# Kernel tuning notes

Measured on AMD Instinct MI355X. Metric: run time of the kernel, lower is better.

The kernel has to match this reference:

```python
import jax, jax.numpy as jnp
import numpy as np

SEQ_LEN, BATCH, VOCAB, EMB, HID, NUM_LAYERS = 128, 64, 10000, 512, 512, 2


def setup_inputs() -> dict:
    key = jax.random.key(0)
    ks = jax.random.split(key, 16)
    b = float(np.sqrt(1.0 / HID))  # Linear init bound per init_weights_uniform
    u = lambda k, shape, bound: jax.random.uniform(k, shape, jnp.float32, -bound, bound)
    L = NUM_LAYERS - 1
    return {
        "inputs": jax.random.randint(ks[0], (SEQ_LEN, BATCH), 0, VOCAB, dtype=jnp.int32),
        "hidden": jnp.zeros((NUM_LAYERS, BATCH, HID), jnp.float32),
        "emb": u(ks[1], (VOCAB, EMB), 0.1),
        "W_ih0": u(ks[2], (HID, EMB), b),
        "b_ih0": u(ks[3], (HID,), b),
        "W_hh0": u(ks[4], (HID, HID), b),
        "b_hh0": u(ks[5], (HID,), b),
        "W_in": u(ks[6], (L, HID, HID), b),
        "b_in": u(ks[7], (L, HID), b),
        "W_hh": u(ks[8], (L, HID, HID), b),
        "b_hh": u(ks[9], (L, HID), b),
        "Wy": u(ks[10], (VOCAB, HID), 0.1),
        "by": jnp.zeros((VOCAB,), jnp.float32),
    }


def reference(inputs, hidden, emb, W_ih0, b_ih0, W_hh0, b_hh0,
              W_in, b_in, W_hh, b_hh, Wy, by):
    n_extra = W_in.shape[0]  # num_layers - 1 (static)

    def step(h, x_t):
        # h: [L, B, H]; x_t: [B] int tokens
        e = emb[x_t]  # [B, E]
        h0 = jnp.tanh(e @ W_ih0.T + b_ih0 + h[0] @ W_hh0.T + b_hh0)
        hs = [h0]
        for l in range(n_extra):  # small static layer loop
            hl = jnp.tanh(hs[-1] @ W_in[l].T + b_in[l]
                          + h[l + 1] @ W_hh[l].T + b_hh[l])
            hs.append(hl)
        h_new = jnp.stack(hs)  # [L, B, H]
        logits_t = hs[-1] @ Wy.T + by  # [B, V]
        return h_new, logits_t

    hidden_final, logits = jax.lax.scan(step, hidden, inputs)
    return logits, hidden_final  # [S, B, V], [L, B, H]
```

## Files before the change

kernel.cpp:

```cpp
#include <hip/hip_runtime.h>
#include <hip/hip_bf16.h>

#define SEQ 128
#define BAT 64
#define VOC 10000
#define EMBD 512
#define HID 512
#define BH (BAT*HID)
#define PRE0_OFF 0
#define H0_OFF   ((size_t)SEQ*BH)
#define H1_OFF   (H0_OFF + (size_t)(SEQ+1)*BH)
#define FLAGS_OFF (H1_OFF + (size_t)(SEQ+1)*BH)
#define CONV_OFF (FLAGS_OFF + 256)
#define LOGITS_N ((size_t)SEQ*BAT*VOC)
#define CONV_USHORTS 5382144ull
#define WS_NEED_FLOATS (CONV_OFF + CONV_USHORTS/2)

typedef __attribute__((ext_vector_type(8))) __bf16 bf16x8;
typedef __attribute__((ext_vector_type(4))) float f32x4;

__global__ __launch_bounds__(256) void init_state_k(const float* __restrict__ hidden,
                                                    float* __restrict__ h0_0,
                                                    float* __restrict__ h1_0,
                                                    unsigned* __restrict__ flags) {
    int i = blockIdx.x * 256 + threadIdx.x;
    if (i < 256) flags[i] = 0u;
    if (i < BH) { h0_0[i] = hidden[i]; h1_0[i] = hidden[BH + i]; }
}

__global__ __launch_bounds__(256) void gemm_nt_k(
    const float* __restrict__ A, const int* __restrict__ tok,
    const float* __restrict__ Bm,
    const float* __restrict__ bias0, const float* __restrict__ bias1,
    float* __restrict__ C, int N, int K, int ldc)
{
    __shared__ float As[32][132];
    __shared__ float Bs[32][132];
    __shared__ int toks[128];

    const int tid = threadIdx.x;
    const int r0 = blockIdx.x * 128;
    const int c0 = blockIdx.y * 128;

    if (tok != nullptr && tid < 128) toks[tid] = tok[r0 + tid];
    __syncthreads();

    const int tn = tid & 15;
    const int tm = tid >> 4;
    const int m0 = tm * 8, n0 = tn * 8;

    float acc[8][8];
#pragma unroll
    for (int i = 0; i < 8; ++i)
#pragma unroll
        for (int j = 0; j < 8; ++j) acc[i][j] = 0.f;

    for (int k0 = 0; k0 < K; k0 += 32) {
#pragma unroll
        for (int p = 0; p < 4; ++p) {
            int idx = p * 256 + tid;
            int row = idx >> 3;
            int kq  = (idx & 7) << 2;
            size_t arow = tok ? (size_t)toks[row] : (size_t)(r0 + row);
            float4 a = *(const float4*)(A + arow * (size_t)K + k0 + kq);
            As[kq+0][row] = a.x; As[kq+1][row] = a.y;
            As[kq+2][row] = a.z; As[kq+3][row] = a.w;
            int gc = c0 + row;
            float4 b = make_float4(0.f, 0.f, 0.f, 0.f);
            if (gc < N) b = *(const float4*)(Bm + (size_t)gc * K + k0 + kq);
            Bs[kq+0][row] = b.x; Bs[kq+1][row] = b.y;
            Bs[kq+2][row] = b.z; Bs[kq+3][row] = b.w;
        }
        __syncthreads();
#pragma unroll 8
        for (int k = 0; k < 32; ++k) {
            float4 a0 = *(const float4*)&As[k][m0];
            float4 a1 = *(const float4*)&As[k][m0 + 4];
            float4 b0 = *(const float4*)&Bs[k][n0];
            float4 b1 = *(const float4*)&Bs[k][n0 + 4];
            float am[8] = {a0.x,a0.y,a0.z,a0.w,a1.x,a1.y,a1.z,a1.w};
            float bn[8] = {b0.x,b0.y,b0.z,b0.w,b1.x,b1.y,b1.z,b1.w};
#pragma unroll
            for (int i = 0; i < 8; ++i)
#pragma unroll
                for (int j = 0; j < 8; ++j) acc[i][j] += am[i] * bn[j];
        }
        __syncthreads();
    }

    const bool full = (c0 + 128 <= N);
#pragma unroll
    for (int i = 0; i < 8; ++i) {
        size_t r = (size_t)(r0 + m0 + i);
        float* crow = C + r * (size_t)ldc;
#pragma unroll
        for (int j = 0; j < 8; ++j) {
            int c = c0 + n0 + j;
            if (full || c < N) {
                float v = acc[i][j];
                if (bias0) v += bias0[c];
                if (bias1) v += bias1[c];
                crow[c] = v;
            }
        }
    }
}

#define BFLY(S, N)                                                     \
    {                                                                  \
        _Pragma("unroll")                                              \
        for (int i = 0; i < N; ++i) {                                  \
            float lo_ = a[i], hi_ = a[i + N];                          \
            float send_ = (lane & S) ? lo_ : hi_;                      \
            float recv_ = __shfl_xor(send_, S);                       \
            a[i] = ((lane & S) ? hi_ : lo_) + recv_;                   \
        }                                                              \
    }

__device__ __forceinline__ unsigned bf16_rne(float x) {
    unsigned u = __float_as_uint(x);
    unsigned r = u + 0x7fffu + ((u >> 16) & 1u);
    return r >> 16;
}

__device__ __forceinline__ void recurrence_body(
    int blk,
    const float* __restrict__ pre0, const float* __restrict__ W_hh0,
    const float* __restrict__ W_in, const float* __restrict__ b_in,
    const float* __restrict__ W_hh, const float* __restrict__ b_hh,
    float* __restrict__ h0_all, float* __restrict__ h1_all,
    unsigned* __restrict__ flags, float* __restrict__ xs)
{
    const int tid  = threadIdx.x;
    const int lane = tid & 63;
    const int wv   = tid >> 6;
    const int p = ((lane&1)<<5)|((lane&2)<<3)|((lane&4)<<1)
                | ((lane&8)>>1)|((lane&16)>>3)|((lane&32)>>5);
    const int b_own = p >> 3, j_own = p & 7;

    unsigned* fl1 = flags;
    unsigned* fl2 = flags + 64;

    float4 wr[8][2];
    float a[64];

    if (blk < 64) {
        const int g = blk >> 4, jb = blk & 15;
        const int bt = wv & 1, jt = wv >> 1;
        const size_t win = (size_t)(g << 4) * HID;
#pragma unroll
        for (int jj = 0; jj < 8; ++jj) {
            const float* wp = W_hh0 + (size_t)(jb*32 + jt*8 + jj) * HID;
            wr[jj][0] = *(const float4*)(wp + lane*4);
            wr[jj][1] = *(const float4*)(wp + 256 + lane*4);
        }
        const unsigned* grp = fl1 + (g << 4);
        unsigned* myf = fl1 + (g << 4) + jb;
        const int bg = (g << 4) + (bt << 3) + b_own;
        const int jg = jb*32 + jt*8 + j_own;

        for (unsigned t = 1; t <= SEQ; ++t) {
            float pf = pre0[(size_t)(t-1)*BH + (size_t)bg*HID + jg];
            for (;;) {
                unsigned v = __hip_atomic_load(&grp[lane & 15], __ATOMIC_RELAXED,
                                               __HIP_MEMORY_SCOPE_AGENT);
                if (__ballot(v < (t - 1)) == 0ull) break;
            }
            __syncthreads();
            {
                const float4* src = (const float4*)(h0_all + (size_t)(t-1)*BH + win);
                float4 r0_, r1_, r2_, r3_;
                asm volatile("global_load_dwordx4 %0, %1, off sc0" : "=v"(r0_) : "v"(src + tid));
                asm volatile("global_load_dwordx4 %0, %1, off sc0" : "=v"(r1_) : "v"(src + tid + 512));
                asm volatile("global_load_dwordx4 %0, %1, off sc0" : "=v"(r2_) : "v"(src + tid + 1024));
                asm volatile("global_load_dwordx4 %0, %1, off sc0" : "=v"(r3_) : "v"(src + tid + 1536));
                asm volatile("s_waitcnt vmcnt(0)" ::: "memory");
                __builtin_amdgcn_sched_barrier(0);
                float4* dst = (float4*)xs;
                dst[tid] = r0_; dst[tid+512] = r1_; dst[tid+1024] = r2_; dst[tid+1536] = r3_;
            }
            __syncthreads();
#pragma unroll
            for (int i = 0; i < 64; ++i) a[i] = 0.f;
#pragma unroll
            for (int b = 0; b < 8; ++b) {
                const int row = (bt << 3) + b;
                float4 ha = *(const float4*)&xs[row*512 + lane*4];
                float4 hb = *(const float4*)&xs[row*512 + 256 + lane*4];
#pragma unroll
                for (int jj = 0; jj < 8; ++jj) {
                    a[b*8+jj] += ha.x*wr[jj][0].x + ha.y*wr[jj][0].y
                               + ha.z*wr[jj][0].z + ha.w*wr[jj][0].w
                               + hb.x*wr[jj][1].x + hb.y*wr[jj][1].y
                               + hb.z*wr[jj][1].z + hb.w*wr[jj][1].w;
                }
            }
            BFLY(1,32) BFLY(2,16) BFLY(4,8) BFLY(8,4) BFLY(16,2) BFLY(32,1)
            float v = tanhf(a[0] + pf);
            __hip_atomic_store(&h0_all[(size_t)t*BH + (size_t)bg*HID + jg], v,
                               __ATOMIC_RELAXED, __HIP_MEMORY_SCOPE_AGENT);
            asm volatile("s_waitcnt vmcnt(0)" ::: "memory");
            __syncthreads();
            if (tid == 0) __hip_atomic_store(myf, t, __ATOMIC_RELAXED,
                                             __HIP_MEMORY_SCOPE_AGENT);
        }
    } else {
        const int idx = blk - 64;
        const int g = idx >> 5, jb = idx & 31;
        const int bt = wv & 1, jt = (wv >> 1) & 1, kt = wv >> 2;
        const size_t win = (size_t)(g << 4) * HID;
        const float* Wmat = kt ? W_hh : W_in;
#pragma unroll
        for (int jj = 0; jj < 8; ++jj) {
            const float* wp = Wmat + (size_t)(jb*16 + jt*8 + jj) * HID;
            wr[jj][0] = *(const float4*)(wp + lane*4);
            wr[jj][1] = *(const float4*)(wp + 256 + lane*4);
        }
        const unsigned* grpA = fl1 + (g << 4);
        const unsigned* grpB = fl2 + (g << 5);
        unsigned* myf = fl2 + (g << 5) + jb;
        const int bg = (g << 4) + (bt << 3) + b_own;
        const int jg = jb*16 + jt*8 + j_own;
        const float bias = b_in[jg] + b_hh[jg];
        const int scx = (wv & 3) * 64 + lane;

        for (unsigned t = 1; t <= SEQ; ++t) {
            for (;;) {
                unsigned v1 = __hip_atomic_load(&grpA[lane & 15], __ATOMIC_RELAXED,
                                                __HIP_MEMORY_SCOPE_AGENT);
                unsigned v2 = __hip_atomic_load(&grpB[lane & 31], __ATOMIC_RELAXED,
                                                __HIP_MEMORY_SCOPE_AGENT);
                if (__ballot(v1 < t) == 0ull && __ballot(v2 < (t - 1)) == 0ull) break;
            }
            __syncthreads();
            {
                const int q = tid & 255;
                const float4* src = (tid < 256)
                    ? (const float4*)(h0_all + (size_t)t*BH + win)
                    : (const float4*)(h1_all + (size_t)(t-1)*BH + win);
                float4 rr[8];
#pragma unroll
                for (int i = 0; i < 8; ++i)
                    asm volatile("global_load_dwordx4 %0, %1, off sc0"
                                 : "=v"(rr[i]) : "v"(src + q + i*256));
                asm volatile("s_waitcnt vmcnt(0)" ::: "memory");
                __builtin_amdgcn_sched_barrier(0);
                float4* dst = (float4*)(xs + ((tid < 256) ? 0 : 8192));
#pragma unroll
                for (int i = 0; i < 8; ++i) dst[q + i*256] = rr[i];
            }
            __syncthreads();
#pragma unroll
            for (int i = 0; i < 64; ++i) a[i] = 0.f;
            const float* xsrc = xs + (kt ? 8192 : 0);
#pragma unroll
            for (int b = 0; b < 8; ++b) {
                const int row = (bt << 3) + b;
                float4 ha = *(const float4*)&xsrc[row*512 + lane*4];
                float4 hb = *(const float4*)&xsrc[row*512 + 256 + lane*4];
#pragma unroll
                for (int jj = 0; jj < 8; ++jj) {
                    a[b*8+jj] += ha.x*wr[jj][0].x + ha.y*wr[jj][0].y
                               + ha.z*wr[jj][0].z + ha.w*wr[jj][0].w
                               + hb.x*wr[jj][1].x + hb.y*wr[jj][1].y
                               + hb.z*wr[jj][1].z + hb.w*wr[jj][1].w;
                }
            }
            BFLY(1,32) BFLY(2,16) BFLY(4,8) BFLY(8,4) BFLY(16,2) BFLY(32,1)
            __syncthreads();
            if (kt) xs[scx] = a[0];
            __syncthreads();
            if (!kt) {
                float v = tanhf(a[0] + xs[scx] + bias);
                __hip_atomic_store(&h1_all[(size_t)t*BH + (size_t)bg*HID + jg], v,
                                   __ATOMIC_RELAXED, __HIP_MEMORY_SCOPE_AGENT);
            }
            asm volatile("s_waitcnt vmcnt(0)" ::: "memory");
            __syncthreads();
            if (tid == 0) __hip_atomic_store(myf, t, __ATOMIC_RELAXED,
                                             __HIP_MEMORY_SCOPE_AGENT);
        }
    }
}

__global__ __launch_bounds__(512) void recurrence_k(
    const float* __restrict__ pre0, const float* __restrict__ W_hh0,
    const float* __restrict__ W_in, const float* __restrict__ b_in,
    const float* __restrict__ W_hh, const float* __restrict__ b_hh,
    float* __restrict__ h0_all, float* __restrict__ h1_all,
    unsigned* __restrict__ flags)
{
    __shared__ float xs[16384];
    recurrence_body(blockIdx.x, pre0, W_hh0, W_in, b_in, W_hh, b_hh,
                    h0_all, h1_all, flags, xs);
}

__global__ __launch_bounds__(512, 2) void recurrence9_k(
    const float* __restrict__ pre0, const float* __restrict__ W_hh0,
    const float* __restrict__ W_in, const float* __restrict__ b_in,
    const float* __restrict__ W_hh, const float* __restrict__ b_hh,
    float* __restrict__ h0_all, float* __restrict__ h1_all,
    unsigned* __restrict__ flags)
{
    __shared__ float xs[16384];
    __shared__ int s_task;

    if (threadIdx.x == 0) {
        unsigned xcc;
        asm volatile("s_getreg_b32 %0, hwreg(20, 0, 4)" : "=s"(xcc));
        unsigned* q = flags + 192;
        int task = -1;
        if (xcc < 4u) {
            unsigned r = atomicAdd(&q[xcc], 1u);
            if (r < 48u) task = (r < 16u) ? (int)(xcc*16u + r)
                                          : (int)(64u + xcc*32u + (r - 16u));
        }
        if (task < 0) {
            __builtin_amdgcn_s_sleep(127);
            for (unsigned g = 0; g < 4u && task < 0; ++g) {
                unsigned r = atomicAdd(&q[g], 1u);
                if (r < 48u) task = (r < 16u) ? (int)(g*16u + r)
                                              : (int)(64u + g*32u + (r - 16u));
            }
        }
        s_task = task;
    }
    __syncthreads();
    const int task = s_task;
    if (task < 0) return;

    recurrence_body(task, pre0, W_hh0, W_in, b_in, W_hh, b_hh,
                    h0_all, h1_all, flags, xs);
}

__global__ __launch_bounds__(256) void copy_out_k(const float* __restrict__ h0_all,
                                                  const float* __restrict__ h1_all,
                                                  float* __restrict__ out_hidden) {
    int g = blockIdx.x * 256 + threadIdx.x;
    if (g < BH)            out_hidden[g] = h0_all[(size_t)SEQ * BH + g];
    else if (g < 2 * BH)   out_hidden[g] = h1_all[(size_t)SEQ * BH + (g - BH)];
}


__global__ __launch_bounds__(256) void split2_hi_k(const float* __restrict__ wy,
                                                   const float* __restrict__ wih0,
                                                   unsigned short* __restrict__ wy_hi,
                                                   unsigned short* __restrict__ wih0_hi) {
    const int n4a = VOC*HID/4;
    const int n4b = HID*EMBD/4;
    int i = blockIdx.x * 256 + threadIdx.x;
    const float* src; unsigned short* dst; int idx;
    if (i < n4a)            { src = wy;   dst = wy_hi;   idx = i; }
    else if (i < n4a + n4b) { src = wih0; dst = wih0_hi; idx = i - n4a; }
    else return;
    float4 v = ((const float4*)src)[idx];
    ushort4 h4;
    h4.x = (unsigned short)bf16_rne(v.x); h4.y = (unsigned short)bf16_rne(v.y);
    h4.z = (unsigned short)bf16_rne(v.z); h4.w = (unsigned short)bf16_rne(v.w);
    ((ushort4*)dst)[idx] = h4;
}

__global__ __launch_bounds__(256) void gemm_mfma2f_k(
    const float* __restrict__ Ag, const int* __restrict__ tok,
    const unsigned short* __restrict__ Bhg,
    const float* __restrict__ bias0, const float* __restrict__ bias1,
    float* __restrict__ C, int N, int ldc)
{
    __shared__ __align__(16) unsigned short sAh[128*64];
    __shared__ __align__(16) unsigned short sAl[128*64];
    __shared__ __align__(16) unsigned short sBh[128*64];

    const int tid = threadIdx.x;
    const int flat = blockIdx.y * gridDim.x + blockIdx.x;
    const int cpx  = (gridDim.x * gridDim.y) >> 3;
    const int w    = (flat & 7) * cpx + (flat >> 3);
    const int r0 = (w & 63) * 128, c0 = (w >> 6) * 128;

    const int lane = tid & 63, wvv = tid >> 6;
    const int mh = wvv >> 1, nh = wvv & 1;

    f32x4 acc[4][4];
#pragma unroll
    for (int i = 0; i < 4; ++i)
#pragma unroll
        for (int j = 0; j < 4; ++j) acc[i][j] = (f32x4){0.f, 0.f, 0.f, 0.f};

    const int srow = tid >> 1, shalf = tid & 1;
    const size_t arow = tok ? (size_t)tok[r0 + srow] : (size_t)(r0 + srow);
    const size_t abase = arow * 512 + (size_t)shalf * 32;
    const int brow = c0 + srow;
    const bool bok = brow < N;
    const size_t bbase = (size_t)(bok ? brow : 0) * 512 + shalf * 32;
    const int woff = srow * 64;
    const int swz = srow & 7;

    float4 fa[4][2];
    uint4 vbh[4];
#pragma unroll
    for (int g = 0; g < 4; ++g) {
        fa[g][0] = *(const float4*)(Ag + abase + g*8);
        fa[g][1] = *(const float4*)(Ag + abase + g*8 + 4);
        vbh[g]   = bok ? *(const uint4*)(Bhg + bbase + g*8) : (uint4){0,0,0,0};
    }

    for (int k0 = 0; k0 < 512; k0 += 64) {
        __syncthreads();
#pragma unroll
        for (int g = 0; g < 4; ++g) {
            float f[8] = {fa[g][0].x, fa[g][0].y, fa[g][0].z, fa[g][0].w,
                          fa[g][1].x, fa[g][1].y, fa[g][1].z, fa[g][1].w};
            unsigned hh[8], ll[8];
#pragma unroll
            for (int q = 0; q < 8; ++q) {
                hh[q] = bf16_rne(f[q]);
                ll[q] = bf16_rne(f[q] - __uint_as_float(hh[q] << 16));
            }
            uint4 ph = { hh[0] | (hh[1]<<16), hh[2] | (hh[3]<<16),
                         hh[4] | (hh[5]<<16), hh[6] | (hh[7]<<16) };
            uint4 pl = { ll[0] | (ll[1]<<16), ll[2] | (ll[3]<<16),
                         ll[4] | (ll[5]<<16), ll[6] | (ll[7]<<16) };
            int off = woff + (((shalf*4 + g) ^ swz) * 8);
            *(uint4*)&sAh[off] = ph;
            *(uint4*)&sAl[off] = pl;
            *(uint4*)&sBh[off] = vbh[g];
        }
        __syncthreads();
        if (k0 < 448) {
            const int kn = k0 + 64;
#pragma unroll
            for (int g = 0; g < 4; ++g) {
                fa[g][0] = *(const float4*)(Ag + abase + kn + g*8);
                fa[g][1] = *(const float4*)(Ag + abase + kn + g*8 + 4);
                vbh[g]   = bok ? *(const uint4*)(Bhg + bbase + kn + g*8) : (uint4){0,0,0,0};
            }
        }
#pragma unroll
        for (int c = 0; c < 2; ++c) {
            const int ks = ((c*4 + (lane >> 4)) ^ (lane & 7)) * 8;
            bf16x8 fAh[4], fAl[4], fBh[4];
#pragma unroll
            for (int mi = 0; mi < 4; ++mi) {
                int ro = (mh*64 + mi*16 + (lane & 15)) * 64;
                fAh[mi] = *(const bf16x8*)&sAh[ro + ks];
                fAl[mi] = *(const bf16x8*)&sAl[ro + ks];
            }
#pragma unroll
            for (int ni = 0; ni < 4; ++ni) {
                int ro = (nh*64 + ni*16 + (lane & 15)) * 64;
                fBh[ni] = *(const bf16x8*)&sBh[ro + ks];
            }
#pragma unroll
            for (int mi = 0; mi < 4; ++mi)
#pragma unroll
                for (int ni = 0; ni < 4; ++ni) {
                    acc[mi][ni] = __builtin_amdgcn_mfma_f32_16x16x32_bf16(
                        fAh[mi], fBh[ni], acc[mi][ni], 0, 0, 0);
                    acc[mi][ni] = __builtin_amdgcn_mfma_f32_16x16x32_bf16(
                        fAl[mi], fBh[ni], acc[mi][ni], 0, 0, 0);
                }
        }
    }

#pragma unroll
    for (int ni = 0; ni < 4; ++ni) {
        int gcol = c0 + nh*64 + ni*16 + (lane & 15);
        bool ok = gcol < N;
        float bias = 0.f;
        if (ok) {
            if (bias0) bias += bias0[gcol];
            if (bias1) bias += bias1[gcol];
        }
#pragma unroll
        for (int mi = 0; mi < 4; ++mi) {
            int grow = r0 + mh*64 + mi*16 + ((lane >> 4) << 2);
#pragma unroll
            for (int r = 0; r < 4; ++r)
                if (ok) C[(size_t)(grow + r) * ldc + gcol] = acc[mi][ni][r] + bias;
        }
    }
}

__global__ __launch_bounds__(256) void gemm_mfma1f_k(
    const float* __restrict__ Ag,
    const unsigned short* __restrict__ Bhg,
    const float* __restrict__ bias0,
    float* __restrict__ C, int N, int ldc)
{
    __shared__ __align__(16) unsigned short sAh[128*64];
    __shared__ __align__(16) unsigned short sBh[128*64];

    const int tid = threadIdx.x;
    const int flat = blockIdx.y * gridDim.x + blockIdx.x;
    const int cpx  = (gridDim.x * gridDim.y) >> 3;
    const int w    = (flat & 7) * cpx + (flat >> 3);
    const int r0 = (w & 63) * 128, c0 = (w >> 6) * 128;

    const int lane = tid & 63, wvv = tid >> 6;
    const int mh = wvv >> 1, nh = wvv & 1;

    f32x4 acc[4][4];
#pragma unroll
    for (int i = 0; i < 4; ++i)
#pragma unroll
        for (int j = 0; j < 4; ++j) acc[i][j] = (f32x4){0.f, 0.f, 0.f, 0.f};

    const int srow = tid >> 1, shalf = tid & 1;
    const size_t abase = (size_t)(r0 + srow) * 512 + (size_t)shalf * 32;
    const int brow = c0 + srow;
    const bool bok = brow < N;
    const size_t bbase = (size_t)(bok ? brow : 0) * 512 + shalf * 32;
    const int woff = srow * 64;
    const int swz = srow & 7;

    float4 fa[4][2];
    uint4 vbh[4];
#pragma unroll
    for (int g = 0; g < 4; ++g) {
        fa[g][0] = *(const float4*)(Ag + abase + g*8);
        fa[g][1] = *(const float4*)(Ag + abase + g*8 + 4);
        vbh[g]   = bok ? *(const uint4*)(Bhg + bbase + g*8) : (uint4){0,0,0,0};
    }

    for (int k0 = 0; k0 < 512; k0 += 64) {
        __syncthreads();
#pragma unroll
        for (int g = 0; g < 4; ++g) {
            float f[8] = {fa[g][0].x, fa[g][0].y, fa[g][0].z, fa[g][0].w,
                          fa[g][1].x, fa[g][1].y, fa[g][1].z, fa[g][1].w};
            unsigned hh[8];
#pragma unroll
            for (int q = 0; q < 8; ++q) hh[q] = bf16_rne(f[q]);
            uint4 ph = { hh[0] | (hh[1]<<16), hh[2] | (hh[3]<<16),
                         hh[4] | (hh[5]<<16), hh[6] | (hh[7]<<16) };
            int off = woff + (((shalf*4 + g) ^ swz) * 8);
            *(uint4*)&sAh[off] = ph;
            *(uint4*)&sBh[off] = vbh[g];
        }
        __syncthreads();
        if (k0 < 448) {
            const int kn = k0 + 64;
#pragma unroll
            for (int g = 0; g < 4; ++g) {
                fa[g][0] = *(const float4*)(Ag + abase + kn + g*8);
                fa[g][1] = *(const float4*)(Ag + abase + kn + g*8 + 4);
                vbh[g]   = bok ? *(const uint4*)(Bhg + bbase + kn + g*8) : (uint4){0,0,0,0};
            }
        }
#pragma unroll
        for (int c = 0; c < 2; ++c) {
            const int ks = ((c*4 + (lane >> 4)) ^ (lane & 7)) * 8;
            bf16x8 fAh[4], fBh[4];
#pragma unroll
            for (int mi = 0; mi < 4; ++mi) {
                int ro = (mh*64 + mi*16 + (lane & 15)) * 64;
                fAh[mi] = *(const bf16x8*)&sAh[ro + ks];
            }
#pragma unroll
            for (int ni = 0; ni < 4; ++ni) {
                int ro = (nh*64 + ni*16 + (lane & 15)) * 64;
                fBh[ni] = *(const bf16x8*)&sBh[ro + ks];
            }
#pragma unroll
            for (int mi = 0; mi < 4; ++mi)
#pragma unroll
                for (int ni = 0; ni < 4; ++ni)
                    acc[mi][ni] = __builtin_amdgcn_mfma_f32_16x16x32_bf16(
                        fAh[mi], fBh[ni], acc[mi][ni], 0, 0, 0);
        }
    }

#pragma unroll
    for (int ni = 0; ni < 4; ++ni) {
        int gcol = c0 + nh*64 + ni*16 + (lane & 15);
        bool ok = gcol < N;
        float bias = ok ? bias0[gcol] : 0.f;
#pragma unroll
        for (int mi = 0; mi < 4; ++mi) {
            int grow = r0 + mh*64 + mi*16 + ((lane >> 4) << 2);
#pragma unroll
            for (int r = 0; r < 4; ++r)
                if (ok) C[(size_t)(grow + r) * ldc + gcol] = acc[mi][ni][r] + bias;
        }
    }
}

extern "C" void kernel_launch(void* const* d_in, const int* in_sizes, int n_in,
                              void* d_out, int out_size, void* d_ws, size_t ws_size,
                              hipStream_t stream) {
    const int*   inputs = (const int*)d_in[0];
    const float* hidden = (const float*)d_in[1];
    const float* emb    = (const float*)d_in[2];
    const float* W_ih0  = (const float*)d_in[3];
    const float* b_ih0  = (const float*)d_in[4];
    const float* W_hh0  = (const float*)d_in[5];
    const float* b_hh0  = (const float*)d_in[6];
    const float* W_in   = (const float*)d_in[7];
    const float* b_in   = (const float*)d_in[8];
    const float* W_hh   = (const float*)d_in[9];
    const float* b_hh   = (const float*)d_in[10];
    const float* Wy     = (const float*)d_in[11];
    const float* by     = (const float*)d_in[12];
    float* out = (float*)d_out;

    float* ws     = (float*)d_ws;
    float* pre0   = ws + PRE0_OFF;
    float* h0_all = ws + H0_OFF;
    float* h1_all = ws + H1_OFF;
    unsigned* flags = (unsigned*)(ws + FLAGS_OFF);
    float* out_hidden = out + LOGITS_N;
    const bool big_ws = (ws_size >= WS_NEED_FLOATS * 4ull);

    unsigned short* wy_hi   = (unsigned short*)(ws + CONV_OFF);
    unsigned short* wih0_hi = wy_hi + (size_t)VOC * HID;

    init_state_k<<<dim3((BH + 255) / 256), dim3(256), 0, stream>>>(hidden, h0_all, h1_all, flags);

    const float* pre0_c = pre0;
    if (big_ws) {
        split2_hi_k<<<dim3((VOC*HID/4 + HID*EMBD/4 + 255) / 256), dim3(256), 0, stream>>>(
            Wy, W_ih0, wy_hi, wih0_hi);
        gemm_mfma2f_k<<<dim3(64, 4), dim3(256), 0, stream>>>(
            emb, inputs, wih0_hi, b_ih0, b_hh0, pre0, HID, HID);

        void* kargs9[] = { (void*)&pre0_c, (void*)&W_hh0, (void*)&W_in, (void*)&b_in,
                           (void*)&W_hh, (void*)&b_hh, (void*)&h0_all, (void*)&h1_all,
                           (void*)&flags };
        hipError_t e = hipLaunchCooperativeKernel((const void*)recurrence9_k,
                                                  dim3(384), dim3(512), kargs9, 0, stream);
        if (e != hipSuccess) {
            (void)hipGetLastError();
            hipLaunchCooperativeKernel((const void*)recurrence_k, dim3(192), dim3(512),
                                       kargs9, 0, stream);
        }

        copy_out_k<<<dim3(256), dim3(256), 0, stream>>>(h0_all, h1_all, out_hidden);
        gemm_mfma1f_k<<<dim3(64, 79), dim3(256), 0, stream>>>(
            h1_all + BH, wy_hi, by, out, VOC, VOC);
    } else {
        gemm_nt_k<<<dim3(64, 4), dim3(256), 0, stream>>>(
            emb, inputs, W_ih0, b_ih0, b_hh0, pre0, HID, EMBD, HID);
        void* kargs[] = { (void*)&pre0_c, (void*)&W_hh0, (void*)&W_in, (void*)&b_in,
                          (void*)&W_hh, (void*)&b_hh, (void*)&h0_all, (void*)&h1_all,
                          (void*)&flags };
        hipLaunchCooperativeKernel((const void*)recurrence_k, dim3(192), dim3(512),
                                   kargs, 0, stream);
        copy_out_k<<<dim3(256), dim3(256), 0, stream>>>(h0_all, h1_all, out_hidden);
        gemm_nt_k<<<dim3(64, 79), dim3(256), 0, stream>>>(
            h1_all + BH, nullptr, Wy, nullptr, by, out, VOC, HID, VOC);
    }
}
```

Measured before the change: 1.118 ms.

## Use per-wave release flags to drop block barriers in recurrence

Each wave now publishes its own progress flag with a release store, and consumers poll all per-wave flags of their group. This removes the trailing vmcnt wait, the __syncthreads before the flag store and one post-spin barrier per step. The change also drops the XCC-aware task assignment kernel in favour of a plain cooperative launch with fixed block mapping. Memory ordering now relies on per-wave release/relaxed polling, which removes serialisation but loses any XCC locality the old mapping gave.

```diff
diff --git a/kernel.cpp b/kernel.cpp
--- a/kernel.cpp
+++ b/kernel.cpp
@@ -11,7 +11,7 @@
 #define H0_OFF   ((size_t)SEQ*BH)
 #define H1_OFF   (H0_OFF + (size_t)(SEQ+1)*BH)
 #define FLAGS_OFF (H1_OFF + (size_t)(SEQ+1)*BH)
-#define CONV_OFF (FLAGS_OFF + 256)
+#define CONV_OFF (FLAGS_OFF + 1024)
 #define LOGITS_N ((size_t)SEQ*BAT*VOC)
 #define CONV_USHORTS 5382144ull
 #define WS_NEED_FLOATS (CONV_OFF + CONV_USHORTS/2)
@@ -24,7 +24,7 @@
                                                     float* __restrict__ h1_0,
                                                     unsigned* __restrict__ flags) {
     int i = blockIdx.x * 256 + threadIdx.x;
-    if (i < 256) flags[i] = 0u;
+    if (i < 1024) flags[i] = 0u;
     if (i < BH) { h0_0[i] = hidden[i]; h1_0[i] = hidden[BH + i]; }
 }
 
@@ -123,14 +123,15 @@
     return r >> 16;
 }
 
-__device__ __forceinline__ void recurrence_body(
-    int blk,
+__global__ __launch_bounds__(512) void recurrence10_k(
     const float* __restrict__ pre0, const float* __restrict__ W_hh0,
     const float* __restrict__ W_in, const float* __restrict__ b_in,
     const float* __restrict__ W_hh, const float* __restrict__ b_hh,
     float* __restrict__ h0_all, float* __restrict__ h1_all,
-    unsigned* __restrict__ flags, float* __restrict__ xs)
+    unsigned* __restrict__ flags)
 {
+    __shared__ float xs[16384 + 256];
+
     const int tid  = threadIdx.x;
     const int lane = tid & 63;
     const int wv   = tid >> 6;
@@ -138,35 +139,33 @@
                 | ((lane&8)>>1)|((lane&16)>>3)|((lane&32)>>5);
     const int b_own = p >> 3, j_own = p & 7;
 
-    unsigned* fl1 = flags;
-    unsigned* fl2 = flags + 64;
-
     float4 wr[8][2];
     float a[64];
 
-    if (blk < 64) {
-        const int g = blk >> 4, jb = blk & 15;
+    if (blockIdx.x < 64) {
+        const int g = blockIdx.x >> 4, jb = blockIdx.x & 15;
         const int bt = wv & 1, jt = wv >> 1;
         const size_t win = (size_t)(g << 4) * HID;
+        unsigned* fl1 = flags + (g << 8);
 #pragma unroll
         for (int jj = 0; jj < 8; ++jj) {
             const float* wp = W_hh0 + (size_t)(jb*32 + jt*8 + jj) * HID;
             wr[jj][0] = *(const float4*)(wp + lane*4);
             wr[jj][1] = *(const float4*)(wp + 256 + lane*4);
         }
-        const unsigned* grp = fl1 + (g << 4);
-        unsigned* myf = fl1 + (g << 4) + jb;
+        unsigned* myf = fl1 + (jb << 3) + wv;
         const int bg = (g << 4) + (bt << 3) + b_own;
         const int jg = jb*32 + jt*8 + j_own;
 
         for (unsigned t = 1; t <= SEQ; ++t) {
             float pf = pre0[(size_t)(t-1)*BH + (size_t)bg*HID + jg];
             for (;;) {
-                unsigned v = __hip_atomic_load(&grp[lane & 15], __ATOMIC_RELAXED,
-                                               __HIP_MEMORY_SCOPE_AGENT);
-                if (__ballot(v < (t - 1)) == 0ull) break;
-            }
-            __syncthreads();
+                unsigned v0 = __hip_atomic_load(&fl1[lane], __ATOMIC_RELAXED,
+                                                __HIP_MEMORY_SCOPE_AGENT);
+                unsigned v1 = __hip_atomic_load(&fl1[lane + 64], __ATOMIC_RELAXED,
+                                                __HIP_MEMORY_SCOPE_AGENT);
+                if (__ballot(v0 < t-1 || v1 < t-1) == 0ull) break;
+            }
             {
                 const float4* src = (const float4*)(h0_all + (size_t)(t-1)*BH + win);
                 float4 r0_, r1_, r2_, r3_;
@@ -199,16 +198,17 @@
             float v = tanhf(a[0] + pf);
             __hip_atomic_store(&h0_all[(size_t)t*BH + (size_t)bg*HID + jg], v,
                                __ATOMIC_RELAXED, __HIP_MEMORY_SCOPE_AGENT);
-            asm volatile("s_waitcnt vmcnt(0)" ::: "memory");
-            __syncthreads();
-            if (tid == 0) __hip_atomic_store(myf, t, __ATOMIC_RELAXED,
-                                             __HIP_MEMORY_SCOPE_AGENT);
+            if (lane == 0)
+                __hip_atomic_store(myf, t, __ATOMIC_RELEASE,
+                                   __HIP_MEMORY_SCOPE_AGENT);
         }
     } else {
-        const int idx = blk - 64;
+        const int idx = blockIdx.x - 64;
         const int g = idx >> 5, jb = idx & 31;
         const int bt = wv & 1, jt = (wv >> 1) & 1, kt = wv >> 2;
         const size_t win = (size_t)(g << 4) * HID;
+        unsigned* fl1 = flags + (g << 8);
+        unsigned* fl2 = fl1 + 128;
         const float* Wmat = kt ? W_hh : W_in;
 #pragma unroll
         for (int jj = 0; jj < 8; ++jj) {
@@ -216,23 +216,25 @@
             wr[jj][0] = *(const float4*)(wp + lane*4);
             wr[jj][1] = *(const float4*)(wp + 256 + lane*4);
         }
-        const unsigned* grpA = fl1 + (g << 4);
-        const unsigned* grpB = fl2 + (g << 5);
-        unsigned* myf = fl2 + (g << 5) + jb;
+        unsigned* myf = fl2 + (jb << 2) + wv;
         const int bg = (g << 4) + (bt << 3) + b_own;
         const int jg = jb*16 + jt*8 + j_own;
         const float bias = b_in[jg] + b_hh[jg];
-        const int scx = (wv & 3) * 64 + lane;
+        const int scx = 16384 + (wv & 3) * 64 + lane;
 
         for (unsigned t = 1; t <= SEQ; ++t) {
             for (;;) {
-                unsigned v1 = __hip_atomic_load(&grpA[lane & 15], __ATOMIC_RELAXED,
+                unsigned a0 = __hip_atomic_load(&fl1[lane], __ATOMIC_RELAXED,
                                                 __HIP_MEMORY_SCOPE_AGENT);
-                unsigned v2 = __hip_atomic_load(&grpB[lane & 31], __ATOMIC_RELAXED,
+                unsigned a1 = __hip_atomic_load(&fl1[lane + 64], __ATOMIC_RELAXED,
                                                 __HIP_MEMORY_SCOPE_AGENT);
-                if (__ballot(v1 < t) == 0ull && __ballot(v2 < (t - 1)) == 0ull) break;
-            }
-            __syncthreads();
+                unsigned b0 = __hip_atomic_load(&fl2[lane], __ATOMIC_RELAXED,
+                                                __HIP_MEMORY_SCOPE_AGENT);
+                unsigned b1 = __hip_atomic_load(&fl2[lane + 64], __ATOMIC_RELAXED,
+                                                __HIP_MEMORY_SCOPE_AGENT);
+                if (__ballot(a0 < t || a1 < t) == 0ull &&
+                    __ballot(b0 < t-1 || b1 < t-1) == 0ull) break;
+            }
             {
                 const int q = tid & 255;
                 const float4* src = (tid < 256)
@@ -267,18 +269,16 @@
                 }
             }
             BFLY(1,32) BFLY(2,16) BFLY(4,8) BFLY(8,4) BFLY(16,2) BFLY(32,1)
-            __syncthreads();
             if (kt) xs[scx] = a[0];
             __syncthreads();
             if (!kt) {
                 float v = tanhf(a[0] + xs[scx] + bias);
                 __hip_atomic_store(&h1_all[(size_t)t*BH + (size_t)bg*HID + jg], v,
                                    __ATOMIC_RELAXED, __HIP_MEMORY_SCOPE_AGENT);
-            }
-            asm volatile("s_waitcnt vmcnt(0)" ::: "memory");
-            __syncthreads();
-            if (tid == 0) __hip_atomic_store(myf, t, __ATOMIC_RELAXED,
-                                             __HIP_MEMORY_SCOPE_AGENT);
+                if (lane == 0)
+                    __hip_atomic_store(myf, t, __ATOMIC_RELEASE,
+                                       __HIP_MEMORY_SCOPE_AGENT);
+            }
         }
     }
 }
@@ -291,46 +291,152 @@
     unsigned* __restrict__ flags)
 {
     __shared__ float xs[16384];
-    recurrence_body(blockIdx.x, pre0, W_hh0, W_in, b_in, W_hh, b_hh,
-                    h0_all, h1_all, flags, xs);
-}
-
-__global__ __launch_bounds__(512, 2) void recurrence9_k(
-    const float* __restrict__ pre0, const float* __restrict__ W_hh0,
-    const float* __restrict__ W_in, const float* __restrict__ b_in,
-    const float* __restrict__ W_hh, const float* __restrict__ b_hh,
-    float* __restrict__ h0_all, float* __restrict__ h1_all,
-    unsigned* __restrict__ flags)
-{
-    __shared__ float xs[16384];
-    __shared__ int s_task;
-
-    if (threadIdx.x == 0) {
-        unsigned xcc;
-        asm volatile("s_getreg_b32 %0, hwreg(20, 0, 4)" : "=s"(xcc));
-        unsigned* q = flags + 192;
-        int task = -1;
-        if (xcc < 4u) {
-            unsigned r = atomicAdd(&q[xcc], 1u);
-            if (r < 48u) task = (r < 16u) ? (int)(xcc*16u + r)
-                                          : (int)(64u + xcc*32u + (r - 16u));
-        }
-        if (task < 0) {
-            __builtin_amdgcn_s_sleep(127);
-            for (unsigned g = 0; g < 4u && task < 0; ++g) {
-                unsigned r = atomicAdd(&q[g], 1u);
-                if (r < 48u) task = (r < 16u) ? (int)(g*16u + r)
-                                              : (int)(64u + g*32u + (r - 16u));
-            }
-        }
-        s_task = task;
-    }
-    __syncthreads();
-    const int task = s_task;
-    if (task < 0) return;
-
-    recurrence_body(task, pre0, W_hh0, W_in, b_in, W_hh, b_hh,
-                    h0_all, h1_all, flags, xs);
+    const int tid  = threadIdx.x;
+    const int lane = tid & 63;
+    const int wv   = tid >> 6;
+    const int p = ((lane&1)<<5)|((lane&2)<<3)|((lane&4)<<1)
+                | ((lane&8)>>1)|((lane&16)>>3)|((lane&32)>>5);
+    const int b_own = p >> 3, j_own = p & 7;
+    unsigned* fl1 = flags;
+    unsigned* fl2 = flags + 64;
+    float4 wr[8][2];
+    float a[64];
+
+    if (blockIdx.x < 64) {
+        const int g = blockIdx.x >> 4, jb = blockIdx.x & 15;
+        const int bt = wv & 1, jt = wv >> 1;
+        const size_t win = (size_t)(g << 4) * HID;
+#pragma unroll
+        for (int jj = 0; jj < 8; ++jj) {
+            const float* wp = W_hh0 + (size_t)(jb*32 + jt*8 + jj) * HID;
+            wr[jj][0] = *(const float4*)(wp + lane*4);
+            wr[jj][1] = *(const float4*)(wp + 256 + lane*4);
+        }
+        const unsigned* grp = fl1 + (g << 4);
+        unsigned* myf = fl1 + (g << 4) + jb;
+        const int bg = (g << 4) + (bt << 3) + b_own;
+        const int jg = jb*32 + jt*8 + j_own;
+        for (unsigned t = 1; t <= SEQ; ++t) {
+            float pf = pre0[(size_t)(t-1)*BH + (size_t)bg*HID + jg];
+            for (;;) {
+                unsigned v = __hip_atomic_load(&grp[lane & 15], __ATOMIC_RELAXED,
+                                               __HIP_MEMORY_SCOPE_AGENT);
+                if (__ballot(v < (t - 1)) == 0ull) break;
+            }
+            __syncthreads();
+            {
+                const float4* src = (const float4*)(h0_all + (size_t)(t-1)*BH + win);
+                float4 r0_, r1_, r2_, r3_;
+                asm volatile("global_load_dwordx4 %0, %1, off sc0" : "=v"(r0_) : "v"(src + tid));
+                asm volatile("global_load_dwordx4 %0, %1, off sc0" : "=v"(r1_) : "v"(src + tid + 512));
+                asm volatile("global_load_dwordx4 %0, %1, off sc0" : "=v"(r2_) : "v"(src + tid + 1024));
+                asm volatile("global_load_dwordx4 %0, %1, off sc0" : "=v"(r3_) : "v"(src + tid + 1536));
+                asm volatile("s_waitcnt vmcnt(0)" ::: "memory");
+                __builtin_amdgcn_sched_barrier(0);
+                float4* dst = (float4*)xs;
+                dst[tid] = r0_; dst[tid+512] = r1_; dst[tid+1024] = r2_; dst[tid+1536] = r3_;
+            }
+            __syncthreads();
+#pragma unroll
+            for (int i = 0; i < 64; ++i) a[i] = 0.f;
+#pragma unroll
+            for (int b = 0; b < 8; ++b) {
+                const int row = (bt << 3) + b;
+                float4 ha = *(const float4*)&xs[row*512 + lane*4];
+                float4 hb = *(const float4*)&xs[row*512 + 256 + lane*4];
+#pragma unroll
+                for (int jj = 0; jj < 8; ++jj) {
+                    a[b*8+jj] += ha.x*wr[jj][0].x + ha.y*wr[jj][0].y
+                               + ha.z*wr[jj][0].z + ha.w*wr[jj][0].w
+                               + hb.x*wr[jj][1].x + hb.y*wr[jj][1].y
+                               + hb.z*wr[jj][1].z + hb.w*wr[jj][1].w;
+                }
+            }
+            BFLY(1,32) BFLY(2,16) BFLY(4,8) BFLY(8,4) BFLY(16,2) BFLY(32,1)
+            float v = tanhf(a[0] + pf);
+            __hip_atomic_store(&h0_all[(size_t)t*BH + (size_t)bg*HID + jg], v,
+                               __ATOMIC_RELAXED, __HIP_MEMORY_SCOPE_AGENT);
+            asm volatile("s_waitcnt vmcnt(0)" ::: "memory");
+            __syncthreads();
+            if (tid == 0) __hip_atomic_store(myf, t, __ATOMIC_RELAXED,
+                                             __HIP_MEMORY_SCOPE_AGENT);
+        }
+    } else {
+        const int idx = blockIdx.x - 64;
+        const int g = idx >> 5, jb = idx & 31;
+        const int bt = wv & 1, jt = (wv >> 1) & 1, kt = wv >> 2;
+        const size_t win = (size_t)(g << 4) * HID;
+        const float* Wmat = kt ? W_hh : W_in;
+#pragma unroll
+        for (int jj = 0; jj < 8; ++jj) {
+            const float* wp = Wmat + (size_t)(jb*16 + jt*8 + jj) * HID;
+            wr[jj][0] = *(const float4*)(wp + lane*4);
+            wr[jj][1] = *(const float4*)(wp + 256 + lane*4);
+        }
+        const unsigned* grpA = fl1 + (g << 4);
+        const unsigned* grpB = fl2 + (g << 5);
+        unsigned* myf = fl2 + (g << 5) + jb;
+        const int bg = (g << 4) + (bt << 3) + b_own;
+        const int jg = jb*16 + jt*8 + j_own;
+        const float bias = b_in[jg] + b_hh[jg];
+        const int scx = (wv & 3) * 64 + lane;
+        for (unsigned t = 1; t <= SEQ; ++t) {
+            for (;;) {
+                unsigned v1 = __hip_atomic_load(&grpA[lane & 15], __ATOMIC_RELAXED,
+                                                __HIP_MEMORY_SCOPE_AGENT);
+                unsigned v2 = __hip_atomic_load(&grpB[lane & 31], __ATOMIC_RELAXED,
+                                                __HIP_MEMORY_SCOPE_AGENT);
+                if (__ballot(v1 < t) == 0ull && __ballot(v2 < (t - 1)) == 0ull) break;
+            }
+            __syncthreads();
+            {
+                const int q = tid & 255;
+                const float4* src = (tid < 256)
+                    ? (const float4*)(h0_all + (size_t)t*BH + win)
+                    : (const float4*)(h1_all + (size_t)(t-1)*BH + win);
+                float4 rr[8];
+#pragma unroll
+                for (int i = 0; i < 8; ++i)
+                    asm volatile("global_load_dwordx4 %0, %1, off sc0"
+                                 : "=v"(rr[i]) : "v"(src + q + i*256));
+                asm volatile("s_waitcnt vmcnt(0)" ::: "memory");
+                __builtin_amdgcn_sched_barrier(0);
+                float4* dst = (float4*)(xs + ((tid < 256) ? 0 : 8192));
+#pragma unroll
+                for (int i = 0; i < 8; ++i) dst[q + i*256] = rr[i];
+            }
+            __syncthreads();
+#pragma unroll
+            for (int i = 0; i < 64; ++i) a[i] = 0.f;
+            const float* xsrc = xs + (kt ? 8192 : 0);
+#pragma unroll
+            for (int b = 0; b < 8; ++b) {
+                const int row = (bt << 3) + b;
+                float4 ha = *(const float4*)&xsrc[row*512 + lane*4];
+                float4 hb = *(const float4*)&xsrc[row*512 + 256 + lane*4];
+#pragma unroll
+                for (int jj = 0; jj < 8; ++jj) {
+                    a[b*8+jj] += ha.x*wr[jj][0].x + ha.y*wr[jj][0].y
+                               + ha.z*wr[jj][0].z + ha.w*wr[jj][0].w
+                               + hb.x*wr[jj][1].x + hb.y*wr[jj][1].y
+                               + hb.z*wr[jj][1].z + hb.w*wr[jj][1].w;
+                }
+            }
+            BFLY(1,32) BFLY(2,16) BFLY(4,8) BFLY(8,4) BFLY(16,2) BFLY(32,1)
+            __syncthreads();
+            if (kt) xs[scx] = a[0];
+            __syncthreads();
+            if (!kt) {
+                float v = tanhf(a[0] + xs[scx] + bias);
+                __hip_atomic_store(&h1_all[(size_t)t*BH + (size_t)bg*HID + jg], v,
+                                   __ATOMIC_RELAXED, __HIP_MEMORY_SCOPE_AGENT);
+            }
+            asm volatile("s_waitcnt vmcnt(0)" ::: "memory");
+            __syncthreads();
+            if (tid == 0) __hip_atomic_store(myf, t, __ATOMIC_RELAXED,
+                                             __HIP_MEMORY_SCOPE_AGENT);
+        }
+    }
 }
 
 __global__ __launch_bounds__(256) void copy_out_k(const float* __restrict__ h0_all,
@@ -622,16 +728,11 @@
         gemm_mfma2f_k<<<dim3(64, 4), dim3(256), 0, stream>>>(
             emb, inputs, wih0_hi, b_ih0, b_hh0, pre0, HID, HID);
 
-        void* kargs9[] = { (void*)&pre0_c, (void*)&W_hh0, (void*)&W_in, (void*)&b_in,
-                           (void*)&W_hh, (void*)&b_hh, (void*)&h0_all, (void*)&h1_all,
-                           (void*)&flags };
-        hipError_t e = hipLaunchCooperativeKernel((const void*)recurrence9_k,
-                                                  dim3(384), dim3(512), kargs9, 0, stream);
-        if (e != hipSuccess) {
-            (void)hipGetLastError();
-            hipLaunchCooperativeKernel((const void*)recurrence_k, dim3(192), dim3(512),
-                                       kargs9, 0, stream);
-        }
+        void* kargs10[] = { (void*)&pre0_c, (void*)&W_hh0, (void*)&W_in, (void*)&b_in,
+                            (void*)&W_hh, (void*)&b_hh, (void*)&h0_all, (void*)&h1_all,
+                            (void*)&flags };
+        hipLaunchCooperativeKernel((const void*)recurrence10_k, dim3(192), dim3(512),
+                                   kargs10, 0, stream);
 
         copy_out_k<<<dim3(256), dim3(256), 0, stream>>>(h0_all, h1_all, out_hidden);
         gemm_mfma1f_k<<<dim3(64, 79), dim3(256), 0, stream>>>(
```

New measurement: 3.633 ms. 225% more time.
